# Performance work log

Hardware: AMD Instinct MI355X
Metric: run time of the kernel (lower is better)

Reference implementation:

```python
import jax, jax.numpy as jnp
import numpy as np

K = 3            # char conv window (in words of chars)
B, P, LC = 64, 80, 18   # batch, padded sentence len, padded word char len
E = 256          # embedding_dim (shared by word and char embeddings)
H = 1024         # lstm hidden
L_CH = 4         # conv output channels
VOCAB, ALPHA, TAGS = 50000, 100, 50


def setup_inputs() -> dict:
    key = jax.random.key(0)
    ks = jax.random.split(key, 12)
    D = E + L_CH  # lstm input dim
    s = 0.02
    return {
        "sentence_batch": jax.random.randint(ks[0], (B, P), 0, VOCAB),
        "character_batch": jax.random.randint(ks[1], (B, P, LC), 0, ALPHA),
        "word_emb": jax.random.normal(ks[2], (VOCAB, E), jnp.float32) * s,
        "char_emb": jax.random.normal(ks[3], (ALPHA, E), jnp.float32) * s,
        "conv_w": jax.random.normal(ks[4], (L_CH, K * E), jnp.float32) * s,
        "conv_b": jax.random.normal(ks[5], (L_CH,), jnp.float32) * s,
        "w_ih": jax.random.normal(ks[6], (4 * H, D), jnp.float32) * s,
        "w_hh": jax.random.normal(ks[7], (4 * H, H), jnp.float32) * s,
        "b_ih": jax.random.normal(ks[8], (4 * H,), jnp.float32) * s,
        "b_hh": jax.random.normal(ks[9], (4 * H,), jnp.float32) * s,
        "out_w": jax.random.normal(ks[10], (TAGS, H), jnp.float32) * s,
        "out_b": jax.random.normal(ks[11], (TAGS,), jnp.float32) * s,
    }


def reference(sentence_batch, character_batch, word_emb, char_emb, conv_w,
              conv_b, w_ih, w_hh, b_ih, b_hh, out_w, out_b):
    # --- char CNN: sliding K-window over char embeddings, flatten, linear, max ---
    ce = char_emb[character_batch]                      # [B,P,LC,E]
    Wn = LC - K + 1                                     # windows per word
    widx = jnp.arange(Wn)[:, None] + jnp.arange(K)      # [Wn,K]
    win = ce[:, :, widx, :].reshape(B, P, Wn, K * E)    # [B,P,Wn,K*E]
    # Conv1d(in=1, out=4, kernel=K*E) on a length-K*E input == one linear per window
    phi = jnp.einsum('bpwd,cd->bpwc', win, conv_w) + conv_b  # [B,P,Wn,4]
    char_repr = phi.max(axis=2)                         # [B,P,4] (max over windows)

    # --- word embeddings + concat ---
    we = word_emb[sentence_batch]                       # [B,P,E]
    combined = jnp.concatenate([we, char_repr], axis=2) # [B,P,E+4]
    D = combined.shape[-1]
    # faithful to torch: .view(PADDING_SIZE, BATCH_SIZE, -1) is a reshape, not transpose
    x = combined.reshape(P, B, D)                       # [P,B,D]

    # --- LSTM (torch gate order i,f,g,o) ---
    def step(carry, x_t):
        h, c = carry
        gates = x_t @ w_ih.T + b_ih + h @ w_hh.T + b_hh  # [B,4H]
        i, f, g, o = jnp.split(gates, 4, axis=-1)
        i = jax.nn.sigmoid(i)
        f = jax.nn.sigmoid(f)
        g = jnp.tanh(g)
        o = jax.nn.sigmoid(o)
        c = f * c + i * g
        h = o * jnp.tanh(c)
        return (h, c), h

    h0 = jnp.zeros((B, H), x.dtype)
    c0 = jnp.zeros((B, H), x.dtype)
    _, hs = jax.lax.scan(step, (h0, c0), x)             # [P,B,H]

    # faithful reshape back, linear head, log_softmax over dim=1 (the P axis)
    lstm_out = hs.reshape(B, P, H)
    tag_space = lstm_out @ out_w.T + out_b              # [B,P,TAGS]
    return jax.nn.log_softmax(tag_space, axis=1)
```

## Files before the change

kernel.cpp:

```cpp
#include <hip/hip_runtime.h>
#include <math.h>

#define BB 64
#define PP 80
#define LC 18
#define EE 256
#define HH 1024
#define LCH 4
#define KW 3
#define TAGS 50
#define DD 260
#define KPAD 288
#define ROWS (BB*PP)
#define WN (LC-KW+1)
#define NG (4*HH)
#define GRP 4
#define UPB 32
#define NBLK (GRP*(HH/UPB))
#define HSTEP32 (GRP*32*512)

typedef __attribute__((ext_vector_type(8))) short short8;
typedef __attribute__((ext_vector_type(4))) short short4v;
typedef __attribute__((ext_vector_type(4))) float floatx4;
typedef __attribute__((ext_vector_type(4))) int int4v;

__device__ __forceinline__ short f2bf(float x) {
    unsigned u = __float_as_uint(x);
    unsigned r = (u + 0x7FFFu + ((u >> 16) & 1u)) >> 16;
    return (short)r;
}
__device__ __forceinline__ float bf2f(short s) {
    return __uint_as_float(((unsigned)(unsigned short)s) << 16);
}
__device__ __forceinline__ float sigf(float x) { return 1.f / (1.f + __expf(-x)); }
__device__ __forceinline__ float tanhfast(float x) {
    float e = __expf(2.f * x);
    return 1.f - 2.f / (e + 1.f);
}
__device__ __forceinline__ float wave_reduce_sum(float v) {
    for (int off = 32; off > 0; off >>= 1) v += __shfl_xor(v, off, 64);
    return v;
}

__global__ __launch_bounds__(256) void prep_kernel(
    const float* __restrict__ wih, const float* __restrict__ whh,
    const float* __restrict__ outw,
    short* __restrict__ wih_bf, short* __restrict__ wpk,
    short* __restrict__ outw_bf, unsigned* __restrict__ hst32)
{
    const int NI = NG * KPAD;
    const int NH = NG * HH;
    const int NO = 64 * HH;
    const int total = NI + NH + NO;
    for (int i = blockIdx.x * 256 + threadIdx.x; i < total; i += gridDim.x * 256) {
        if (i < NI) {
            int r = i / KPAD, c = i - r * KPAD;
            wih_bf[i] = (c < DD) ? f2bf(wih[r * DD + c]) : (short)0;
        } else if (i < NI + NH) {
            int o = i - NI;
            int e  = o & 7;
            int l  = (o >> 3) & 63;
            int s  = (o >> 9) & 3;
            int tl = (o >> 11) & 7;
            int w  = (o >> 14) & 7;
            int bl = o >> 17;
            int row = (tl >> 1) * HH + bl * 32 + (tl & 1) * 16 + (l & 15);
            int col = w * 128 + s * 32 + (l >> 4) * 8 + e;
            wpk[o] = f2bf(whh[(size_t)row * HH + col]);
        } else {
            int k = i - NI - NH;
            int r = k >> 10;
            outw_bf[k] = (r < TAGS) ? f2bf(outw[k]) : (short)0;
        }
    }
    int4v z = {0, 0, 0, 0};
    int4v* hz = (int4v*)hst32;
    const int NZ = PP * HSTEP32 / 4;
    for (int i = blockIdx.x * 256 + threadIdx.x; i < NZ; i += gridDim.x * 256)
        hz[i] = z;
}

__global__ __launch_bounds__(256) void embed_kernel(
    const int* __restrict__ sent, const int* __restrict__ chars,
    const float* __restrict__ word_emb, const float* __restrict__ char_emb,
    const float* __restrict__ conv_w, const float* __restrict__ conv_b,
    short* __restrict__ X)
{
    __shared__ float4 ce[LC * 64];
    __shared__ float phi[WN * LCH];
    __shared__ float charrep[LCH];
    const int r = blockIdx.x;
    const int t = threadIdx.x;
    const int lane = t & 63, wv = t >> 6;

    const int cbase = r * LC;
    for (int i = 0; i < 5; ++i) {
        int idx = i * 256 + t;
        if (idx < LC * 64) {
            int j = idx >> 6, e4 = idx & 63;
            int ch = chars[cbase + j];
            ce[idx] = ((const float4*)(char_emb + (size_t)ch * EE))[e4];
        }
    }
    float4 cw[KW][LCH];
    #pragma unroll
    for (int k = 0; k < KW; ++k)
        #pragma unroll
        for (int c = 0; c < LCH; ++c)
            cw[k][c] = ((const float4*)(conv_w + c * (KW * EE) + k * EE))[lane];
    __syncthreads();

    #pragma unroll
    for (int wi = 0; wi < 4; ++wi) {
        int w = wv + wi * 4;
        float acc[LCH] = {0.f, 0.f, 0.f, 0.f};
        #pragma unroll
        for (int k = 0; k < KW; ++k) {
            float4 v = ce[(w + k) * 64 + lane];
            #pragma unroll
            for (int c = 0; c < LCH; ++c)
                acc[c] += v.x * cw[k][c].x + v.y * cw[k][c].y +
                          v.z * cw[k][c].z + v.w * cw[k][c].w;
        }
        #pragma unroll
        for (int c = 0; c < LCH; ++c) {
            float s = wave_reduce_sum(acc[c]);
            if (lane == 0) phi[w * LCH + c] = s;
        }
    }
    __syncthreads();
    if (t < LCH) {
        float m = -1e30f;
        for (int w = 0; w < WN; ++w) m = fmaxf(m, phi[w * LCH + t]);
        charrep[t] = m + conv_b[t];
    }
    __syncthreads();

    const int word = sent[r];
    X[(size_t)r * KPAD + t] = f2bf(word_emb[(size_t)word * EE + t]);
    if (t < LCH) X[(size_t)r * KPAD + EE + t] = f2bf(charrep[t]);
    if (t >= 228) X[(size_t)r * KPAD + 32 + t] = (short)0;
}

__global__ __launch_bounds__(256) void gemm_in_kernel(
    const short* __restrict__ X, const short* __restrict__ Wih,
    const float* __restrict__ b_ih, const float* __restrict__ b_hh,
    short* __restrict__ ginP)
{
    const int tid = threadIdx.x;
    const int l = tid & 63, wv = tid >> 6;
    const int r0 = blockIdx.x * 64;
    const int n0 = blockIdx.y * 128 + wv * 32;
    const int lr = l & 15, lh = l >> 4;

    floatx4 acc[4][2];
    #pragma unroll
    for (int m = 0; m < 4; ++m)
        #pragma unroll
        for (int n = 0; n < 2; ++n) acc[m][n] = (floatx4)0.f;

    const short* Xb = X + (size_t)(r0 + lr) * KPAD + lh * 8;
    const short* Wb = Wih + (size_t)(n0 + lr) * KPAD + lh * 8;

    #pragma unroll
    for (int k0 = 0; k0 < KPAD; k0 += 32) {
        short8 a0 = *(const short8*)(Xb + k0);
        short8 a1 = *(const short8*)(Xb + 16 * KPAD + k0);
        short8 a2 = *(const short8*)(Xb + 32 * KPAD + k0);
        short8 a3 = *(const short8*)(Xb + 48 * KPAD + k0);
        short8 b0 = *(const short8*)(Wb + k0);
        short8 b1 = *(const short8*)(Wb + 16 * KPAD + k0);
        acc[0][0] = __builtin_amdgcn_mfma_f32_16x16x32_bf16(a0, b0, acc[0][0], 0, 0, 0);
        acc[1][0] = __builtin_amdgcn_mfma_f32_16x16x32_bf16(a1, b0, acc[1][0], 0, 0, 0);
        acc[2][0] = __builtin_amdgcn_mfma_f32_16x16x32_bf16(a2, b0, acc[2][0], 0, 0, 0);
        acc[3][0] = __builtin_amdgcn_mfma_f32_16x16x32_bf16(a3, b0, acc[3][0], 0, 0, 0);
        acc[0][1] = __builtin_amdgcn_mfma_f32_16x16x32_bf16(a0, b1, acc[0][1], 0, 0, 0);
        acc[1][1] = __builtin_amdgcn_mfma_f32_16x16x32_bf16(a1, b1, acc[1][1], 0, 0, 0);
        acc[2][1] = __builtin_amdgcn_mfma_f32_16x16x32_bf16(a2, b1, acc[2][1], 0, 0, 0);
        acc[3][1] = __builtin_amdgcn_mfma_f32_16x16x32_bf16(a3, b1, acc[3][1], 0, 0, 0);
    }
    #pragma unroll
    for (int m = 0; m < 4; ++m)
        #pragma unroll
        for (int n = 0; n < 2; ++n) {
            int col = n0 + n * 16 + lr;
            float bias = b_ih[col] + b_hh[col];
            short4v pack;
            #pragma unroll
            for (int q = 0; q < 4; ++q) pack[q] = f2bf(acc[m][n][q] + bias);
            int w_ = col >> 10, bl_ = (col >> 4) & 63, uu_ = col & 15;
            size_t addr = ((((size_t)(blockIdx.x * GRP + m) * 64 + bl_) * 4 + w_) * 16
                           + uu_) * 16 + lh * 4;
            *(short4v*)(ginP + addr) = pack;
        }
}

__global__ __launch_bounds__(512, 1) void lstm_seq_kernel(
    unsigned* __restrict__ hst, const short* __restrict__ wpk,
    const short* __restrict__ ginP)
{
    __shared__ __align__(16) float lds_g[8][8][16][20];
    __shared__ __align__(16) unsigned hbuf32[64][12];

    const int tid = threadIdx.x;
    const int l = tid & 63;
    const int w = tid >> 6;
    const int g  = blockIdx.x >> 5;
    const int bl = blockIdx.x & 31;

    short8 barr[8][4];
    {
        const short* wb = wpk + (size_t)(bl * 8 + w) * 16384 + l * 8;
        #pragma unroll
        for (int tl = 0; tl < 8; ++tl)
            #pragma unroll
            for (int s = 0; s < 4; ++s)
                barr[tl][s] = *(const short8*)(wb + tl * 2048 + s * 512);
    }

    const int b16 = tid & 15;
    const int uu  = tid >> 4;
    const int U_  = bl * 32 + uu;
    float c = 0.f;

    float gv[4];
    {
        const short* gb = ginP + (((size_t)g * 64 + (U_ >> 4)) * 4) * 256
                          + (U_ & 15) * 16 + b16;
        #pragma unroll
        for (int q = 0; q < 4; ++q) gv[q] = bf2f(gb[q * 256]);
    }

    for (int t = 0; t < PP; ++t) {
        if (t > 0) {
            const unsigned* A = hst + (size_t)(t - 1) * HSTEP32 + g * 16384
                                + (w * 4) * 512 + l * 8;
            int4v d[8];
            unsigned stale = 0xFu;
            do {
                #pragma unroll
                for (int s = 0; s < 4; ++s)
                    if (stale & (1u << s)) {
                        asm volatile("global_load_dwordx4 %0, %1, off sc0 sc1"
                                     : "=v"(d[2 * s]) : "v"(A + s * 512) : "memory");
                        asm volatile("global_load_dwordx4 %0, %1, off sc0 sc1"
                                     : "=v"(d[2 * s + 1]) : "v"(A + s * 512 + 4) : "memory");
                    }
                asm volatile("s_waitcnt vmcnt(0)" ::: "memory");
                __builtin_amdgcn_sched_barrier(0);
                #pragma unroll
                for (int s = 0; s < 4; ++s)
                    if (stale & (1u << s)) {
                        int ok = 1;
                        #pragma unroll
                        for (int i = 0; i < 2; ++i)
                            #pragma unroll
                            for (int j = 0; j < 4; ++j)
                                ok &= ((((unsigned)d[2 * s + i][j]) & 0xFFFFu)
                                       == (unsigned)t);
                        if (__all(ok)) stale &= ~(1u << s);
                    }
                if (stale) __builtin_amdgcn_s_sleep(1);
            } while (stale);

            floatx4 acc[8];
            #pragma unroll
            for (int tl = 0; tl < 8; ++tl) acc[tl] = (floatx4)0.f;
            #pragma unroll
            for (int s = 0; s < 4; ++s) {
                int4v pk;
                pk[0] = (int)((((unsigned)d[2*s][0]) >> 16)   | (((unsigned)d[2*s][1])   & 0xFFFF0000u));
                pk[1] = (int)((((unsigned)d[2*s][2]) >> 16)   | (((unsigned)d[2*s][3])   & 0xFFFF0000u));
                pk[2] = (int)((((unsigned)d[2*s+1][0]) >> 16) | (((unsigned)d[2*s+1][1]) & 0xFFFF0000u));
                pk[3] = (int)((((unsigned)d[2*s+1][2]) >> 16) | (((unsigned)d[2*s+1][3]) & 0xFFFF0000u));
                short8 av = __builtin_bit_cast(short8, pk);
                #pragma unroll
                for (int tl = 0; tl < 8; ++tl)
                    acc[tl] = __builtin_amdgcn_mfma_f32_16x16x32_bf16(
                        av, barr[tl][s], acc[tl], 0, 0, 0);
            }
            #pragma unroll
            for (int tl = 0; tl < 8; ++tl)
                *(floatx4*)&lds_g[w][tl][l & 15][(l >> 4) * 4] = acc[tl];
            __syncthreads();
        }

        {
            float s0 = gv[0], s1 = gv[1], s2 = gv[2], s3 = gv[3];
            if (t > 0) {
                #pragma unroll
                for (int w2 = 0; w2 < 8; ++w2) {
                    s0 += lds_g[w2][0 + (uu >> 4)][uu & 15][b16];
                    s1 += lds_g[w2][2 + (uu >> 4)][uu & 15][b16];
                    s2 += lds_g[w2][4 + (uu >> 4)][uu & 15][b16];
                    s3 += lds_g[w2][6 + (uu >> 4)][uu & 15][b16];
                }
            }
            float i_ = sigf(s0), f_ = sigf(s1), g_ = tanhfast(s2), o_ = sigf(s3);
            c = f_ * c + i_ * g_;
            unsigned hd = (((unsigned)(unsigned short)f2bf(o_ * tanhfast(c))) << 16)
                          | (unsigned)(t + 1);
            hbuf32[(uu >> 3) * 16 + b16][uu & 7] = hd;

            if (t + 1 < PP) {
                const short* gb = ginP + ((((size_t)(t + 1) * GRP + g) * 64
                                          + (U_ >> 4)) * 4) * 256 + (U_ & 15) * 16 + b16;
                #pragma unroll
                for (int q = 0; q < 4; ++q) gv[q] = bf2f(gb[q * 256]);
            }
        }
        __syncthreads();

        if (tid < 128) {
            int lane_ = tid >> 1, e0 = (tid & 1) * 4;
            int4v hv = *(const int4v*)&hbuf32[lane_][e0];
            unsigned* hp = hst + (size_t)t * HSTEP32 + g * 16384 + bl * 512
                           + lane_ * 8 + e0;
            asm volatile("global_store_dwordx4 %0, %1, off sc0 sc1"
                         :: "v"(hp), "v"(hv) : "memory");
        }
    }
}

__global__ __launch_bounds__(256) void tag_kernel(
    const unsigned* __restrict__ hst, const short* __restrict__ outw_bf,
    const float* __restrict__ out_b, float* __restrict__ out)
{
    const int tid = threadIdx.x;
    const int l = tid & 63, wv = tid >> 6;
    const int t = blockIdx.x;
    const int n0 = wv * 16;
    const int lr = l & 15, lh = l >> 4;

    const unsigned* At = hst + (size_t)t * HSTEP32;
    const short* Bw = outw_bf + (size_t)(n0 + lr) * HH + lh * 8;

    floatx4 acc[4];
    #pragma unroll
    for (int m = 0; m < 4; ++m) acc[m] = (floatx4)0.f;

    #pragma unroll 4
    for (int kk = 0; kk < 32; ++kk) {
        short8 b = *(const short8*)(Bw + kk * 32);
        #pragma unroll
        for (int m = 0; m < 4; ++m) {
            const unsigned* ap = At + m * 16384 + kk * 512 + l * 8;
            int4v d0 = *(const int4v*)(ap);
            int4v d1 = *(const int4v*)(ap + 4);
            int4v pk;
            pk[0] = (int)((((unsigned)d0[0]) >> 16) | (((unsigned)d0[1]) & 0xFFFF0000u));
            pk[1] = (int)((((unsigned)d0[2]) >> 16) | (((unsigned)d0[3]) & 0xFFFF0000u));
            pk[2] = (int)((((unsigned)d1[0]) >> 16) | (((unsigned)d1[1]) & 0xFFFF0000u));
            pk[3] = (int)((((unsigned)d1[2]) >> 16) | (((unsigned)d1[3]) & 0xFFFF0000u));
            short8 a = __builtin_bit_cast(short8, pk);
            acc[m] = __builtin_amdgcn_mfma_f32_16x16x32_bf16(a, b, acc[m], 0, 0, 0);
        }
    }
    int col = n0 + lr;
    if (col < TAGS) {
        float bias = out_b[col];
        #pragma unroll
        for (int m = 0; m < 4; ++m)
            #pragma unroll
            for (int q = 0; q < 4; ++q) {
                int row = t * 64 + m * 16 + lh * 4 + q;
                out[(size_t)row * TAGS + col] = acc[m][q] + bias;
            }
    }
}

__global__ __launch_bounds__(256) void logsoftmax_kernel(float* __restrict__ out)
{
    const int tid = threadIdx.x;
    const int lane = tid & 63;
    const int pair = blockIdx.x * 4 + (tid >> 6);
    if (pair >= BB * TAGS) return;
    const int bb = pair / TAGS, g = pair % TAGS;
    float* base = out + (size_t)bb * PP * TAGS + g;
    float v0 = base[lane * TAGS];
    float v1 = (lane < PP - 64) ? base[(lane + 64) * TAGS] : -1e30f;
    float m = fmaxf(v0, v1);
    for (int off = 32; off > 0; off >>= 1) m = fmaxf(m, __shfl_xor(m, off, 64));
    float s = __expf(v0 - m) + ((lane < PP - 64) ? __expf(v1 - m) : 0.f);
    s = wave_reduce_sum(s);
    float lz = m + __logf(s);
    base[lane * TAGS] = v0 - lz;
    if (lane < PP - 64) base[(lane + 64) * TAGS] = v1 - lz;
}

extern "C" void kernel_launch(void* const* d_in, const int* in_sizes, int n_in,
                              void* d_out, int out_size, void* d_ws, size_t ws_size,
                              hipStream_t stream)
{
    const int*   sent     = (const int*)d_in[0];
    const int*   chars    = (const int*)d_in[1];
    const float* word_emb = (const float*)d_in[2];
    const float* char_emb = (const float*)d_in[3];
    const float* conv_w   = (const float*)d_in[4];
    const float* conv_b   = (const float*)d_in[5];
    const float* w_ih     = (const float*)d_in[6];
    const float* w_hh     = (const float*)d_in[7];
    const float* b_ih     = (const float*)d_in[8];
    const float* b_hh     = (const float*)d_in[9];
    const float* out_w    = (const float*)d_in[10];
    const float* out_b    = (const float*)d_in[11];
    float* out = (float*)d_out;

    short* X_bf     = (short*)d_ws;
    short* wih_bf   = X_bf + (size_t)ROWS * KPAD;
    short* wpk      = wih_bf + (size_t)NG * KPAD;
    short* outw_bf  = wpk + (size_t)NG * HH;
    short* ginP     = outw_bf + (size_t)64 * HH;
    unsigned* hst32 = (unsigned*)(ginP + (size_t)NG * ROWS);

    hipLaunchKernelGGL(prep_kernel, dim3(2048), dim3(256), 0, stream,
                       w_ih, w_hh, out_w, wih_bf, wpk, outw_bf, hst32);
    hipLaunchKernelGGL(embed_kernel, dim3(ROWS), dim3(256), 0, stream,
                       sent, chars, word_emb, char_emb, conv_w, conv_b, X_bf);
    hipLaunchKernelGGL(gemm_in_kernel, dim3(ROWS / 64, NG / 128), dim3(256), 0, stream,
                       X_bf, wih_bf, b_ih, b_hh, ginP);
    {
        void* kargs[3] = { (void*)&hst32, (void*)&wpk, (void*)&ginP };
        hipLaunchCooperativeKernel((void*)lstm_seq_kernel, dim3(NBLK), dim3(512),
                                   kargs, 0, stream);
    }
    hipLaunchKernelGGL(tag_kernel, dim3(PP), dim3(256), 0, stream,
                       hst32, outw_bf, out_b, out);
    hipLaunchKernelGGL(logsoftmax_kernel, dim3((BB * TAGS + 3) / 4), dim3(256), 0, stream,
                       out);
}
```

Measured before the change: 463.8 us.

## Fuse input projection into LSTM recurrence and fuse tag head with log-softmax

Removes the separate input-projection GEMM: each LSTM block keeps its W_ih slice in LDS and computes its x_t·W_ih gate contribution per step with MFMA, issuing the h-state poll loads beforehand so the projection overlaps the wait on other blocks. The tag linear layer and log-softmax are merged into one kernel per batch row that holds the logits in LDS. This drops two launches and the round trip of the large precomputed gate buffer through memory, at the cost of extra per-step compute and LDS use on the serial recurrence path.

```diff
diff --git a/kernel.cpp b/kernel.cpp
--- a/kernel.cpp
+++ b/kernel.cpp
@@ -142,64 +142,14 @@
     if (t >= 228) X[(size_t)r * KPAD + 32 + t] = (short)0;
 }
 
-__global__ __launch_bounds__(256) void gemm_in_kernel(
-    const short* __restrict__ X, const short* __restrict__ Wih,
-    const float* __restrict__ b_ih, const float* __restrict__ b_hh,
-    short* __restrict__ ginP)
-{
-    const int tid = threadIdx.x;
-    const int l = tid & 63, wv = tid >> 6;
-    const int r0 = blockIdx.x * 64;
-    const int n0 = blockIdx.y * 128 + wv * 32;
-    const int lr = l & 15, lh = l >> 4;
-
-    floatx4 acc[4][2];
-    #pragma unroll
-    for (int m = 0; m < 4; ++m)
-        #pragma unroll
-        for (int n = 0; n < 2; ++n) acc[m][n] = (floatx4)0.f;
-
-    const short* Xb = X + (size_t)(r0 + lr) * KPAD + lh * 8;
-    const short* Wb = Wih + (size_t)(n0 + lr) * KPAD + lh * 8;
-
-    #pragma unroll
-    for (int k0 = 0; k0 < KPAD; k0 += 32) {
-        short8 a0 = *(const short8*)(Xb + k0);
-        short8 a1 = *(const short8*)(Xb + 16 * KPAD + k0);
-        short8 a2 = *(const short8*)(Xb + 32 * KPAD + k0);
-        short8 a3 = *(const short8*)(Xb + 48 * KPAD + k0);
-        short8 b0 = *(const short8*)(Wb + k0);
-        short8 b1 = *(const short8*)(Wb + 16 * KPAD + k0);
-        acc[0][0] = __builtin_amdgcn_mfma_f32_16x16x32_bf16(a0, b0, acc[0][0], 0, 0, 0);
-        acc[1][0] = __builtin_amdgcn_mfma_f32_16x16x32_bf16(a1, b0, acc[1][0], 0, 0, 0);
-        acc[2][0] = __builtin_amdgcn_mfma_f32_16x16x32_bf16(a2, b0, acc[2][0], 0, 0, 0);
-        acc[3][0] = __builtin_amdgcn_mfma_f32_16x16x32_bf16(a3, b0, acc[3][0], 0, 0, 0);
-        acc[0][1] = __builtin_amdgcn_mfma_f32_16x16x32_bf16(a0, b1, acc[0][1], 0, 0, 0);
-        acc[1][1] = __builtin_amdgcn_mfma_f32_16x16x32_bf16(a1, b1, acc[1][1], 0, 0, 0);
-        acc[2][1] = __builtin_amdgcn_mfma_f32_16x16x32_bf16(a2, b1, acc[2][1], 0, 0, 0);
-        acc[3][1] = __builtin_amdgcn_mfma_f32_16x16x32_bf16(a3, b1, acc[3][1], 0, 0, 0);
-    }
-    #pragma unroll
-    for (int m = 0; m < 4; ++m)
-        #pragma unroll
-        for (int n = 0; n < 2; ++n) {
-            int col = n0 + n * 16 + lr;
-            float bias = b_ih[col] + b_hh[col];
-            short4v pack;
-            #pragma unroll
-            for (int q = 0; q < 4; ++q) pack[q] = f2bf(acc[m][n][q] + bias);
-            int w_ = col >> 10, bl_ = (col >> 4) & 63, uu_ = col & 15;
-            size_t addr = ((((size_t)(blockIdx.x * GRP + m) * 64 + bl_) * 4 + w_) * 16
-                           + uu_) * 16 + lh * 4;
-            *(short4v*)(ginP + addr) = pack;
-        }
-}
-
 __global__ __launch_bounds__(512, 1) void lstm_seq_kernel(
     unsigned* __restrict__ hst, const short* __restrict__ wpk,
-    const short* __restrict__ ginP)
-{
-    __shared__ __align__(16) float lds_g[8][8][16][20];
+    const short* __restrict__ wih_bf, const short* __restrict__ X,
+    const float* __restrict__ b_ih, const float* __restrict__ b_hh)
+{
+    __shared__ __align__(16) float lds_g[8][8][16][16];
+    __shared__ __align__(16) float lds_gin[8][16][17];
+    __shared__ __align__(16) short Wlds[8][9][64][8];
     __shared__ __align__(16) unsigned hbuf32[64][12];
 
     const int tid = threadIdx.x;
@@ -218,34 +168,55 @@
                 barr[tl][s] = *(const short8*)(wb + tl * 2048 + s * 512);
     }
 
+    float bias_v;
+    {
+        int rr = w * 16 + (l & 15);
+        int grow = (rr >> 5) * HH + bl * 32 + (rr & 31);
+        const short* src = wih_bf + (size_t)grow * KPAD + (l >> 4) * 8;
+        #pragma unroll
+        for (int ks = 0; ks < 9; ++ks)
+            *(short8*)&Wlds[w][ks][l][0] = *(const short8*)(src + ks * 32);
+        bias_v = b_ih[grow] + b_hh[grow];
+    }
+
     const int b16 = tid & 15;
     const int uu  = tid >> 4;
-    const int U_  = bl * 32 + uu;
     float c = 0.f;
 
-    float gv[4];
-    {
-        const short* gb = ginP + (((size_t)g * 64 + (U_ >> 4)) * 4) * 256
-                          + (U_ & 15) * 16 + b16;
-        #pragma unroll
-        for (int q = 0; q < 4; ++q) gv[q] = bf2f(gb[q * 256]);
-    }
-
     for (int t = 0; t < PP; ++t) {
+        int4v d[8];
         if (t > 0) {
             const unsigned* A = hst + (size_t)(t - 1) * HSTEP32 + g * 16384
                                 + (w * 4) * 512 + l * 8;
-            int4v d[8];
+            #pragma unroll
+            for (int s = 0; s < 4; ++s) {
+                asm volatile("global_load_dwordx4 %0, %1, off sc0 sc1"
+                             : "=v"(d[2 * s]) : "v"(A + s * 512) : "memory");
+                asm volatile("global_load_dwordx4 %0, %1, off sc0 sc1"
+                             : "=v"(d[2 * s + 1]) : "v"(A + s * 512 + 4) : "memory");
+            }
+        }
+
+        {
+            floatx4 gacc = (floatx4)0.f;
+            const short* Xrow = X + ((size_t)t * 64 + g * 16 + (l & 15)) * KPAD
+                                + (l >> 4) * 8;
+            #pragma unroll
+            for (int ks = 0; ks < 9; ++ks) {
+                short8 a  = *(const short8*)(Xrow + ks * 32);
+                short8 bf = *(const short8*)&Wlds[w][ks][l][0];
+                gacc = __builtin_amdgcn_mfma_f32_16x16x32_bf16(a, bf, gacc, 0, 0, 0);
+            }
+            #pragma unroll
+            for (int q = 0; q < 4; ++q)
+                lds_gin[w][(l >> 4) * 4 + q][l & 15] = gacc[q] + bias_v;
+        }
+
+        if (t > 0) {
+            const unsigned* A = hst + (size_t)(t - 1) * HSTEP32 + g * 16384
+                                + (w * 4) * 512 + l * 8;
             unsigned stale = 0xFu;
-            do {
-                #pragma unroll
-                for (int s = 0; s < 4; ++s)
-                    if (stale & (1u << s)) {
-                        asm volatile("global_load_dwordx4 %0, %1, off sc0 sc1"
-                                     : "=v"(d[2 * s]) : "v"(A + s * 512) : "memory");
-                        asm volatile("global_load_dwordx4 %0, %1, off sc0 sc1"
-                                     : "=v"(d[2 * s + 1]) : "v"(A + s * 512 + 4) : "memory");
-                    }
+            for (;;) {
                 asm volatile("s_waitcnt vmcnt(0)" ::: "memory");
                 __builtin_amdgcn_sched_barrier(0);
                 #pragma unroll
@@ -260,8 +231,17 @@
                                        == (unsigned)t);
                         if (__all(ok)) stale &= ~(1u << s);
                     }
-                if (stale) __builtin_amdgcn_s_sleep(1);
-            } while (stale);
+                if (!stale) break;
+                __builtin_amdgcn_s_sleep(1);
+                #pragma unroll
+                for (int s = 0; s < 4; ++s)
+                    if (stale & (1u << s)) {
+                        asm volatile("global_load_dwordx4 %0, %1, off sc0 sc1"
+                                     : "=v"(d[2 * s]) : "v"(A + s * 512) : "memory");
+                        asm volatile("global_load_dwordx4 %0, %1, off sc0 sc1"
+                                     : "=v"(d[2 * s + 1]) : "v"(A + s * 512 + 4) : "memory");
+                    }
+            }
 
             floatx4 acc[8];
             #pragma unroll
@@ -282,11 +262,14 @@
             #pragma unroll
             for (int tl = 0; tl < 8; ++tl)
                 *(floatx4*)&lds_g[w][tl][l & 15][(l >> 4) * 4] = acc[tl];
-            __syncthreads();
-        }
+        }
+        __syncthreads();
 
         {
-            float s0 = gv[0], s1 = gv[1], s2 = gv[2], s3 = gv[3];
+            float s0 = lds_gin[0 + (uu >> 4)][b16][uu & 15];
+            float s1 = lds_gin[2 + (uu >> 4)][b16][uu & 15];
+            float s2 = lds_gin[4 + (uu >> 4)][b16][uu & 15];
+            float s3 = lds_gin[6 + (uu >> 4)][b16][uu & 15];
             if (t > 0) {
                 #pragma unroll
                 for (int w2 = 0; w2 < 8; ++w2) {
@@ -301,13 +284,6 @@
             unsigned hd = (((unsigned)(unsigned short)f2bf(o_ * tanhfast(c))) << 16)
                           | (unsigned)(t + 1);
             hbuf32[(uu >> 3) * 16 + b16][uu & 7] = hd;
-
-            if (t + 1 < PP) {
-                const short* gb = ginP + ((((size_t)(t + 1) * GRP + g) * 64
-                                          + (U_ >> 4)) * 4) * 256 + (U_ & 15) * 16 + b16;
-                #pragma unroll
-                for (int q = 0; q < 4; ++q) gv[q] = bf2f(gb[q * 256]);
-            }
         }
         __syncthreads();
 
@@ -322,29 +298,31 @@
     }
 }
 
-__global__ __launch_bounds__(256) void tag_kernel(
+__global__ __launch_bounds__(256) void tagsm_kernel(
     const unsigned* __restrict__ hst, const short* __restrict__ outw_bf,
     const float* __restrict__ out_b, float* __restrict__ out)
 {
+    __shared__ float sm[PP][52];
+    __shared__ float lzb[64];
     const int tid = threadIdx.x;
     const int l = tid & 63, wv = tid >> 6;
-    const int t = blockIdx.x;
-    const int n0 = wv * 16;
+    const int b = blockIdx.x;
     const int lr = l & 15, lh = l >> 4;
 
-    const unsigned* At = hst + (size_t)t * HSTEP32;
-    const short* Bw = outw_bf + (size_t)(n0 + lr) * HH + lh * 8;
-
-    floatx4 acc[4];
+    const short* Bw = outw_bf + (size_t)(wv * 16 + lr) * HH + lh * 8;
+
+    floatx4 acc[5];
     #pragma unroll
-    for (int m = 0; m < 4; ++m) acc[m] = (floatx4)0.f;
-
-    #pragma unroll 4
+    for (int m = 0; m < 5; ++m) acc[m] = (floatx4)0.f;
+
     for (int kk = 0; kk < 32; ++kk) {
-        short8 b = *(const short8*)(Bw + kk * 32);
-        #pragma unroll
-        for (int m = 0; m < 4; ++m) {
-            const unsigned* ap = At + m * 16384 + kk * 512 + l * 8;
+        short8 bfr = *(const short8*)(Bw + kk * 32);
+        #pragma unroll
+        for (int m = 0; m < 5; ++m) {
+            int q = b * PP + m * 16 + lr;
+            int t = q >> 6, gg = (q >> 4) & 3, b16 = q & 15;
+            const unsigned* ap = hst + (size_t)t * HSTEP32 + gg * 16384
+                                 + kk * 512 + (lh * 16 + b16) * 8;
             int4v d0 = *(const int4v*)(ap);
             int4v d1 = *(const int4v*)(ap + 4);
             int4v pk;
@@ -353,39 +331,33 @@
             pk[2] = (int)((((unsigned)d1[0]) >> 16) | (((unsigned)d1[1]) & 0xFFFF0000u));
             pk[3] = (int)((((unsigned)d1[2]) >> 16) | (((unsigned)d1[3]) & 0xFFFF0000u));
             short8 a = __builtin_bit_cast(short8, pk);
-            acc[m] = __builtin_amdgcn_mfma_f32_16x16x32_bf16(a, b, acc[m], 0, 0, 0);
-        }
-    }
-    int col = n0 + lr;
+            acc[m] = __builtin_amdgcn_mfma_f32_16x16x32_bf16(a, bfr, acc[m], 0, 0, 0);
+        }
+    }
+    int col = wv * 16 + lr;
     if (col < TAGS) {
         float bias = out_b[col];
         #pragma unroll
-        for (int m = 0; m < 4; ++m)
-            #pragma unroll
-            for (int q = 0; q < 4; ++q) {
-                int row = t * 64 + m * 16 + lh * 4 + q;
-                out[(size_t)row * TAGS + col] = acc[m][q] + bias;
-            }
-    }
-}
-
-__global__ __launch_bounds__(256) void logsoftmax_kernel(float* __restrict__ out)
-{
-    const int tid = threadIdx.x;
-    const int lane = tid & 63;
-    const int pair = blockIdx.x * 4 + (tid >> 6);
-    if (pair >= BB * TAGS) return;
-    const int bb = pair / TAGS, g = pair % TAGS;
-    float* base = out + (size_t)bb * PP * TAGS + g;
-    float v0 = base[lane * TAGS];
-    float v1 = (lane < PP - 64) ? base[(lane + 64) * TAGS] : -1e30f;
-    float m = fmaxf(v0, v1);
-    for (int off = 32; off > 0; off >>= 1) m = fmaxf(m, __shfl_xor(m, off, 64));
-    float s = __expf(v0 - m) + ((lane < PP - 64) ? __expf(v1 - m) : 0.f);
-    s = wave_reduce_sum(s);
-    float lz = m + __logf(s);
-    base[lane * TAGS] = v0 - lz;
-    if (lane < PP - 64) base[(lane + 64) * TAGS] = v1 - lz;
+        for (int m = 0; m < 5; ++m)
+            #pragma unroll
+            for (int q4 = 0; q4 < 4; ++q4)
+                sm[m * 16 + lh * 4 + q4][col] = acc[m][q4] + bias;
+    }
+    __syncthreads();
+
+    if (tid < TAGS) {
+        float mx = -1e30f;
+        for (int p = 0; p < PP; ++p) mx = fmaxf(mx, sm[p][tid]);
+        float s = 0.f;
+        for (int p = 0; p < PP; ++p) s += __expf(sm[p][tid] - mx);
+        lzb[tid] = mx + __logf(s);
+    }
+    __syncthreads();
+
+    for (int idx = tid; idx < PP * TAGS; idx += 256) {
+        int p = idx / TAGS, j = idx - p * TAGS;
+        out[(size_t)b * (PP * TAGS) + idx] = sm[p][j] - lzb[j];
+    }
 }
 
 extern "C" void kernel_launch(void* const* d_in, const int* in_sizes, int n_in,
@@ -410,22 +382,18 @@
     short* wih_bf   = X_bf + (size_t)ROWS * KPAD;
     short* wpk      = wih_bf + (size_t)NG * KPAD;
     short* outw_bf  = wpk + (size_t)NG * HH;
-    short* ginP     = outw_bf + (size_t)64 * HH;
-    unsigned* hst32 = (unsigned*)(ginP + (size_t)NG * ROWS);
+    unsigned* hst32 = (unsigned*)(outw_bf + (size_t)64 * HH);
 
     hipLaunchKernelGGL(prep_kernel, dim3(2048), dim3(256), 0, stream,
                        w_ih, w_hh, out_w, wih_bf, wpk, outw_bf, hst32);
     hipLaunchKernelGGL(embed_kernel, dim3(ROWS), dim3(256), 0, stream,
                        sent, chars, word_emb, char_emb, conv_w, conv_b, X_bf);
-    hipLaunchKernelGGL(gemm_in_kernel, dim3(ROWS / 64, NG / 128), dim3(256), 0, stream,
-                       X_bf, wih_bf, b_ih, b_hh, ginP);
     {
-        void* kargs[3] = { (void*)&hst32, (void*)&wpk, (void*)&ginP };
+        void* kargs[6] = { (void*)&hst32, (void*)&wpk, (void*)&wih_bf,
+                           (void*)&X_bf, (void*)&b_ih, (void*)&b_hh };
         hipLaunchCooperativeKernel((void*)lstm_seq_kernel, dim3(NBLK), dim3(512),
                                    kargs, 0, stream);
     }
-    hipLaunchKernelGGL(tag_kernel, dim3(PP), dim3(256), 0, stream,
+    hipLaunchKernelGGL(tagsm_kernel, dim3(BB), dim3(256), 0, stream,
                        hst32, outw_bf, out_b, out);
-    hipLaunchKernelGGL(logsoftmax_kernel, dim3((BB * TAGS + 3) / 4), dim3(256), 0, stream,
-                       out);
-}
+}
```

Result: slower. 511.7 us (+10.3%).

## Store LSTM h directly per thread and fuse tag head with log-softmax

Applied to the files above, without the earlier changes.

In the recurrent kernel each thread now writes its h/flag word straight to global memory with a coherent dword store. This replaces the LDS staging buffer and the vectorized store issued by the first 128 threads after the barrier, so h is published earlier in each step at the cost of many narrow stores. Separately, the tag projection and log-softmax over P are fused into one kernel with one block per batch row. That block computes all 80 positions into shared memory, reduces over P there and writes the final output, removing a kernel launch and a round trip through global memory.

```diff
diff --git a/kernel.cpp b/kernel.cpp
--- a/kernel.cpp
+++ b/kernel.cpp
@@ -200,7 +200,6 @@
     const short* __restrict__ ginP)
 {
     __shared__ __align__(16) float lds_g[8][8][16][20];
-    __shared__ __align__(16) unsigned hbuf32[64][12];
 
     const int tid = threadIdx.x;
     const int l = tid & 63;
@@ -222,6 +221,9 @@
     const int uu  = tid >> 4;
     const int U_  = bl * 32 + uu;
     float c = 0.f;
+
+    const size_t hoff = (size_t)g * 16384 + bl * 512
+                        + ((uu >> 3) * 16 + b16) * 8 + (uu & 7);
 
     float gv[4];
     {
@@ -300,7 +302,9 @@
             c = f_ * c + i_ * g_;
             unsigned hd = (((unsigned)(unsigned short)f2bf(o_ * tanhfast(c))) << 16)
                           | (unsigned)(t + 1);
-            hbuf32[(uu >> 3) * 16 + b16][uu & 7] = hd;
+            unsigned* hp = hst + (size_t)t * HSTEP32 + hoff;
+            asm volatile("global_store_dword %0, %1, off sc0 sc1"
+                         :: "v"(hp), "v"(hd) : "memory");
 
             if (t + 1 < PP) {
                 const short* gb = ginP + ((((size_t)(t + 1) * GRP + g) * 64
@@ -310,41 +314,34 @@
             }
         }
         __syncthreads();
-
-        if (tid < 128) {
-            int lane_ = tid >> 1, e0 = (tid & 1) * 4;
-            int4v hv = *(const int4v*)&hbuf32[lane_][e0];
-            unsigned* hp = hst + (size_t)t * HSTEP32 + g * 16384 + bl * 512
-                           + lane_ * 8 + e0;
-            asm volatile("global_store_dwordx4 %0, %1, off sc0 sc1"
-                         :: "v"(hp), "v"(hv) : "memory");
-        }
-    }
-}
-
-__global__ __launch_bounds__(256) void tag_kernel(
+    }
+}
+
+__global__ __launch_bounds__(256) void tagsm_kernel(
     const unsigned* __restrict__ hst, const short* __restrict__ outw_bf,
     const float* __restrict__ out_b, float* __restrict__ out)
 {
+    __shared__ float sm[PP][52];
+    __shared__ float lzb[64];
     const int tid = threadIdx.x;
     const int l = tid & 63, wv = tid >> 6;
-    const int t = blockIdx.x;
-    const int n0 = wv * 16;
+    const int b = blockIdx.x;
     const int lr = l & 15, lh = l >> 4;
 
-    const unsigned* At = hst + (size_t)t * HSTEP32;
-    const short* Bw = outw_bf + (size_t)(n0 + lr) * HH + lh * 8;
-
-    floatx4 acc[4];
-    #pragma unroll
-    for (int m = 0; m < 4; ++m) acc[m] = (floatx4)0.f;
-
-    #pragma unroll 4
+    const short* Bw = outw_bf + (size_t)(wv * 16 + lr) * HH + lh * 8;
+
+    floatx4 acc[5];
+    #pragma unroll
+    for (int m = 0; m < 5; ++m) acc[m] = (floatx4)0.f;
+
     for (int kk = 0; kk < 32; ++kk) {
-        short8 b = *(const short8*)(Bw + kk * 32);
-        #pragma unroll
-        for (int m = 0; m < 4; ++m) {
-            const unsigned* ap = At + m * 16384 + kk * 512 + l * 8;
+        short8 bfr = *(const short8*)(Bw + kk * 32);
+        #pragma unroll
+        for (int m = 0; m < 5; ++m) {
+            int q = b * PP + m * 16 + lr;
+            int t = q >> 6, gg = (q >> 4) & 3, b16 = q & 15;
+            const unsigned* ap = hst + (size_t)t * HSTEP32 + gg * 16384
+                                 + kk * 512 + (lh * 16 + b16) * 8;
             int4v d0 = *(const int4v*)(ap);
             int4v d1 = *(const int4v*)(ap + 4);
             int4v pk;
@@ -353,39 +350,33 @@
             pk[2] = (int)((((unsigned)d1[0]) >> 16) | (((unsigned)d1[1]) & 0xFFFF0000u));
             pk[3] = (int)((((unsigned)d1[2]) >> 16) | (((unsigned)d1[3]) & 0xFFFF0000u));
             short8 a = __builtin_bit_cast(short8, pk);
-            acc[m] = __builtin_amdgcn_mfma_f32_16x16x32_bf16(a, b, acc[m], 0, 0, 0);
-        }
-    }
-    int col = n0 + lr;
+            acc[m] = __builtin_amdgcn_mfma_f32_16x16x32_bf16(a, bfr, acc[m], 0, 0, 0);
+        }
+    }
+    int col = wv * 16 + lr;
     if (col < TAGS) {
         float bias = out_b[col];
         #pragma unroll
-        for (int m = 0; m < 4; ++m)
-            #pragma unroll
-            for (int q = 0; q < 4; ++q) {
-                int row = t * 64 + m * 16 + lh * 4 + q;
-                out[(size_t)row * TAGS + col] = acc[m][q] + bias;
-            }
-    }
-}
-
-__global__ __launch_bounds__(256) void logsoftmax_kernel(float* __restrict__ out)
-{
-    const int tid = threadIdx.x;
-    const int lane = tid & 63;
-    const int pair = blockIdx.x * 4 + (tid >> 6);
-    if (pair >= BB * TAGS) return;
-    const int bb = pair / TAGS, g = pair % TAGS;
-    float* base = out + (size_t)bb * PP * TAGS + g;
-    float v0 = base[lane * TAGS];
-    float v1 = (lane < PP - 64) ? base[(lane + 64) * TAGS] : -1e30f;
-    float m = fmaxf(v0, v1);
-    for (int off = 32; off > 0; off >>= 1) m = fmaxf(m, __shfl_xor(m, off, 64));
-    float s = __expf(v0 - m) + ((lane < PP - 64) ? __expf(v1 - m) : 0.f);
-    s = wave_reduce_sum(s);
-    float lz = m + __logf(s);
-    base[lane * TAGS] = v0 - lz;
-    if (lane < PP - 64) base[(lane + 64) * TAGS] = v1 - lz;
+        for (int m = 0; m < 5; ++m)
+            #pragma unroll
+            for (int q4 = 0; q4 < 4; ++q4)
+                sm[m * 16 + lh * 4 + q4][col] = acc[m][q4] + bias;
+    }
+    __syncthreads();
+
+    if (tid < TAGS) {
+        float mx = -1e30f;
+        for (int p = 0; p < PP; ++p) mx = fmaxf(mx, sm[p][tid]);
+        float s = 0.f;
+        for (int p = 0; p < PP; ++p) s += __expf(sm[p][tid] - mx);
+        lzb[tid] = mx + __logf(s);
+    }
+    __syncthreads();
+
+    for (int idx = tid; idx < PP * TAGS; idx += 256) {
+        int p = idx / TAGS, j = idx - p * TAGS;
+        out[(size_t)b * (PP * TAGS) + idx] = sm[p][j] - lzb[j];
+    }
 }
 
 extern "C" void kernel_launch(void* const* d_in, const int* in_sizes, int n_in,
@@ -424,8 +415,6 @@
         hipLaunchCooperativeKernel((void*)lstm_seq_kernel, dim3(NBLK), dim3(512),
                                    kargs, 0, stream);
     }
-    hipLaunchKernelGGL(tag_kernel, dim3(PP), dim3(256), 0, stream,
+    hipLaunchKernelGGL(tagsm_kernel, dim3(BB), dim3(256), 0, stream,
                        hst32, outw_bf, out_b, out);
-    hipLaunchKernelGGL(logsoftmax_kernel, dim3((BB * TAGS + 3) / 4), dim3(256), 0, stream,
-                       out);
-}
+}
```

Result: faster. 417.3 us (-10.0%).
